# Performance work log

Hardware: AMD Instinct MI355X
Metric: run time of the kernel (lower is better)

## Reference

```python
import jax, jax.numpy as jnp
import numpy as np

B, S, D, H, HD = 2, 2048, 2048, 16, 128
MAX_TIMESCALE = 10000.0


def _fixed_pos_embedding(features, length, max_timescale):
    # flaxformer embedding.generate_fixed_pos_embedding
    fraction = jnp.arange(0, features, 2, dtype=jnp.float32) / features
    timescale = max_timescale ** fraction  # min_timescale = 1.0
    sinusoid = jnp.einsum('i,j->ij', jnp.arange(length, dtype=jnp.float32), 1.0 / timescale)
    sinusoid = jnp.concatenate([sinusoid, sinusoid], axis=-1)  # [length, features]
    return jnp.sin(sinusoid), jnp.cos(sinusoid)


def _rotate_half(x):
    x1, x2 = jnp.split(x, 2, axis=-1)
    return jnp.concatenate([-x2, x1], axis=-1)


def _apply_rope(x, sin, cos):
    # x: [B, S, H, HD]; sin/cos: [S, HD]
    sin = sin[None, :, None, :].astype(x.dtype)
    cos = cos[None, :, None, :].astype(x.dtype)
    return x * cos + _rotate_half(x) * sin


def setup_inputs() -> dict:
    key = jax.random.key(0)
    ks = jax.random.split(key, 6)
    inputs_q = jax.random.normal(ks[0], (B, S, D), dtype=jnp.float32)
    inputs_kv = jax.random.normal(ks[1], (B, S, D), dtype=jnp.float32)
    scale = D ** -0.5
    wq = jax.random.normal(ks[2], (D, H, HD), dtype=jnp.float32) * scale
    wk = jax.random.normal(ks[3], (D, H, HD), dtype=jnp.float32) * scale
    wv = jax.random.normal(ks[4], (D, H, HD), dtype=jnp.float32) * scale
    wo = jax.random.normal(ks[5], (H, HD, D), dtype=jnp.float32) * ((H * HD) ** -0.5)
    mask = jnp.tril(jnp.ones((S, S), dtype=bool))[None, None]  # causal [1,1,S,S]
    return {"inputs_q": inputs_q, "inputs_kv": inputs_kv, "wq": wq, "wk": wk,
            "wv": wv, "wo": wo, "mask": mask}


def reference(inputs_q, inputs_kv, wq, wk, wv, wo, mask):
    # QKV projections (split-head kernels) -> [B, S, H, HD]
    q = jnp.einsum('bqd,dhf->bqhf', inputs_q, wq)
    k = jnp.einsum('bkd,dhf->bkhf', inputs_kv, wk)
    v = jnp.einsum('bkd,dhf->bkhf', inputs_kv, wv)

    # Rotary embeddings applied to full head dim (fraction_to_rotate = 1.0)
    sin, cos = _fixed_pos_embedding(HD, S, MAX_TIMESCALE)
    q = _apply_rope(q, sin, cos)
    k = _apply_rope(k, sin, cos)

    # Logit rescaling by 1/sqrt(head_dim) (rescale_logits=False default path)
    q = q * (HD ** -0.5)

    logits = jnp.einsum('bqhf,bkhf->bhqk', q, k)  # [B, H, S, S]
    logits = jnp.where(mask, logits, jnp.asarray(-1e10, logits.dtype))
    probs = jax.nn.softmax(logits, axis=-1)

    ctx = jnp.einsum('bhqk,bkhf->bqhf', probs, v)
    out = jnp.einsum('bqhf,hfd->bqd', ctx, wo)  # output projection
    return out
```

## Files before the change

kernel.cpp:

```cpp
#include <hip/hip_runtime.h>

#define S_LEN 2048
#define NH 16
#define HDIM 128
#define DMODEL 2048

typedef __attribute__((ext_vector_type(8))) short bf16x8;
typedef __attribute__((ext_vector_type(4))) float f32x4;

using gas_cvp = const __attribute__((address_space(1))) void*;
using las_vp  = __attribute__((address_space(3))) void*;

__device__ __forceinline__ unsigned short f2bf(float x) {
  unsigned int u = __builtin_bit_cast(unsigned int, x);
  u += 0x7FFFu + ((u >> 16) & 1u);
  return (unsigned short)(u >> 16);
}
__device__ __forceinline__ float bf2f(unsigned short u) {
  unsigned int x = ((unsigned int)u) << 16;
  return __builtin_bit_cast(float, x);
}
__device__ __forceinline__ unsigned int cvt_pk_bf16(float lo, float hi) {
  unsigned int r;
  asm("v_cvt_pk_bf16_f32 %0, %1, %2" : "=v"(r) : "v"(lo), "v"(hi));
  return r;
}

__global__ __launch_bounds__(256) void cvt_kernel(const float4* __restrict__ in,
                                                  ushort4* __restrict__ out, int n4) {
  int i = blockIdx.x * 256 + threadIdx.x;
  if (i < n4) {
    float4 v = in[i];
    ushort4 r;
    r.x = f2bf(v.x); r.y = f2bf(v.y); r.z = f2bf(v.z); r.w = f2bf(v.w);
    out[i] = r;
  }
}

__global__ __launch_bounds__(256) void sincos_kernel(float2* __restrict__ sc) {
  int i = blockIdx.x * 256 + threadIdx.x;
  int s = i >> 6, j = i & 63;
  float inv_ts = 1.0f / powf(10000.0f, (float)j * (1.0f / 64.0f));
  float ang = (float)s * inv_ts;
  sc[i] = make_float2(sinf(ang), cosf(ang));
}

__global__ __launch_bounds__(256) void rope8_kernel(const unsigned short* __restrict__ X,
                                                    const float2* __restrict__ sc,
                                                    unsigned short* __restrict__ out,
                                                    float scale) {
  int i = blockIdx.x * 256 + threadIdx.x;
  int m = i >> 7;
  int r = i & 127;
  int h = r >> 3, jb = (r & 7) * 8;
  int s = m & (S_LEN - 1);
  size_t base = (size_t)m * DMODEL + h * HDIM + jb;
  int4 x1 = *(const int4*)(X + base);
  int4 x2 = *(const int4*)(X + base + 64);
  const float2* pp = sc + s * 64 + jb;
  int4 o1, o2;
  int* x1w = (int*)&x1; int* x2w = (int*)&x2;
  int* o1w = (int*)&o1; int* o2w = (int*)&o2;
#pragma unroll
  for (int w = 0; w < 4; w++) {
    float a_lo = bf2f((unsigned short)(x1w[w] & 0xffff));
    float a_hi = bf2f((unsigned short)((unsigned int)x1w[w] >> 16));
    float b_lo = bf2f((unsigned short)(x2w[w] & 0xffff));
    float b_hi = bf2f((unsigned short)((unsigned int)x2w[w] >> 16));
    float2 c0 = pp[w * 2], c1 = pp[w * 2 + 1];
    float r1l = (a_lo * c0.y - b_lo * c0.x) * scale;
    float r1h = (a_hi * c1.y - b_hi * c1.x) * scale;
    float r2l = (b_lo * c0.y + a_lo * c0.x) * scale;
    float r2h = (b_hi * c1.y + a_hi * c1.x) * scale;
    o1w[w] = (int)(cvt_pk_bf16(r1l, r1h));
    o2w[w] = (int)(cvt_pk_bf16(r2l, r2h));
  }
  *(int4*)(out + base) = o1;
  *(int4*)(out + base + 64) = o2;
}

__global__ __launch_bounds__(256) void wtrans_kernel(const float* __restrict__ in,
                                                     unsigned short* __restrict__ out) {
  __shared__ float tile[64][65];
  int c0 = blockIdx.x * 64, r0 = blockIdx.y * 64;
  int tx = threadIdx.x & 63, ty = threadIdx.x >> 6;
#pragma unroll
  for (int i = 0; i < 16; i++) {
    int r = ty + i * 4;
    tile[r][tx] = in[(size_t)(r0 + r) * DMODEL + c0 + tx];
  }
  __syncthreads();
#pragma unroll
  for (int i = 0; i < 16; i++) {
    int c = ty + i * 4;
    out[(size_t)(c0 + c) * DMODEL + r0 + tx] = f2bf(tile[tx][c]);
  }
}

__global__ __launch_bounds__(256) void vtrans_kernel(const unsigned short* __restrict__ vf,
                                                     unsigned short* __restrict__ Vt) {
  __shared__ unsigned short tile[64][65];
  int z = blockIdx.z; int b = z >> 4, h = z & 15;
  const unsigned short* I = vf + (size_t)b * S_LEN * DMODEL + h * HDIM;
  unsigned short* O = Vt + (size_t)z * HDIM * S_LEN;
  int s0 = blockIdx.y * 64, f0 = blockIdx.x * 64;
  int tx = threadIdx.x & 63, ty = threadIdx.x >> 6;
#pragma unroll
  for (int i = 0; i < 16; i++) {
    int r = ty + i * 4;
    tile[r][tx] = I[(size_t)(s0 + r) * DMODEL + f0 + tx];
  }
  __syncthreads();
#pragma unroll
  for (int i = 0; i < 16; i++) {
    int c = ty + i * 4;
    O[(size_t)(f0 + c) * S_LEN + s0 + tx] = tile[tx][c];
  }
}

template <bool BF16OUT>
__global__ __launch_bounds__(512) void gemm3b_kernel(
    const unsigned short* __restrict__ Aq,
    const unsigned short* __restrict__ Akv,
    const unsigned short* __restrict__ W,
    void* __restrict__ Cb) {
  constexpr int M = 4096, N = 2048, K = 2048, NT = K / 64;
  __shared__ char lds[147456];
  int z = blockIdx.z;
  const unsigned short* A = (z == 0) ? Aq : Akv;
  const unsigned short* Bt = W + (size_t)z * N * K;

  int wid = blockIdx.y * 16 + blockIdx.x;
  int nid = (wid & 7) * 32 + (wid >> 3);
  int bn = (nid & 15) * 128, bm = (nid >> 4) * 256;

  int tid = threadIdx.x, wave = tid >> 6, lane = tid & 63;
  int lr = lane & 15, lq = lane >> 4;
  int wr = wave >> 1, wc = wave & 1;

  auto STAGE_U = [&](int t, int buf, int which) {
    int k0 = (t & (NT - 1)) * 64;
    const unsigned short* src = (which < 2) ? A : Bt;
    int rbase = (which < 2) ? (bm + which * 128) : bn;
    char* dst0 = lds + buf * 49152 + which * 16384;
#pragma unroll
    for (int i = 0; i < 2; i++) {
      int o = i * 8192 + wave * 1024 + lane * 16;
      int row = o >> 7, colb = o & 127;
      int sc = colb ^ ((row & 7) << 4);
      __builtin_amdgcn_global_load_lds(
          (gas_cvp)(src + (size_t)(rbase + row) * K + k0 + (sc >> 1)),
          (las_vp)(dst0 + i * 8192 + wave * 1024), 16, 0, 0);
    }
  };
  auto LDA = [&](int buf, int m, int kk) -> bf16x8 {
    int row = wr * 64 + m * 16 + lr;
    int half = row >> 7, r = row & 127;
    int byt = r * 128 + (((kk * 4 + lq) ^ (r & 7)) << 4);
    return *(const bf16x8*)(lds + buf * 49152 + half * 16384 + byt);
  };
  auto LDB = [&](int buf, int n, int kk) -> bf16x8 {
    int row = wc * 64 + n * 16 + lr;
    int byt = row * 128 + (((kk * 4 + lq) ^ (row & 7)) << 4);
    return *(const bf16x8*)(lds + buf * 49152 + 32768 + byt);
  };

  f32x4 acc[4][4] = {};
  bf16x8 aA[2][2], bB[4][2];

  auto MFMA_H = [&](int mg) {
#pragma unroll
    for (int kk = 0; kk < 2; kk++)
#pragma unroll
      for (int mm = 0; mm < 2; mm++)
#pragma unroll
        for (int nn = 0; nn < 4; nn++)
          acc[mg * 2 + mm][nn] = __builtin_amdgcn_mfma_f32_16x16x32_bf16(
              aA[mm][kk], bB[nn][kk], acc[mg * 2 + mm][nn], 0, 0, 0);
  };
  auto PHASE_SYNC = [&]() {
    __builtin_amdgcn_s_barrier();
    asm volatile("s_waitcnt lgkmcnt(0)" ::: "memory");
    __builtin_amdgcn_sched_barrier(0);
    __builtin_amdgcn_s_setprio(1);
  };
  auto PHASE_END = [&]() {
    __builtin_amdgcn_s_setprio(0);
    __builtin_amdgcn_s_barrier();
  };

  STAGE_U(0, 0, 0); STAGE_U(0, 0, 1); STAGE_U(0, 0, 2);
  STAGE_U(1, 1, 0); STAGE_U(1, 1, 1); STAGE_U(1, 1, 2);
  asm volatile("s_waitcnt vmcnt(6)" ::: "memory");
  __builtin_amdgcn_sched_barrier(0);
  __builtin_amdgcn_s_barrier();

  int cur = 0;
  for (int T = 0; T < NT; T++) {
    int t2 = (T + 2) & (NT - 1);
    int b2 = cur + 2; if (b2 >= 3) b2 -= 3;
#pragma unroll
    for (int kk = 0; kk < 2; kk++) {
#pragma unroll
      for (int mm = 0; mm < 2; mm++) aA[mm][kk] = LDA(cur, mm, kk);
#pragma unroll
      for (int nn = 0; nn < 4; nn++) bB[nn][kk] = LDB(cur, nn, kk);
    }
    STAGE_U(t2, b2, 2); STAGE_U(t2, b2, 0);
    PHASE_SYNC(); MFMA_H(0); PHASE_END();

#pragma unroll
    for (int kk = 0; kk < 2; kk++)
#pragma unroll
      for (int mm = 0; mm < 2; mm++) aA[mm][kk] = LDA(cur, 2 + mm, kk);
    STAGE_U(t2, b2, 1);
    asm volatile("s_waitcnt vmcnt(6)" ::: "memory");
    __builtin_amdgcn_sched_barrier(0);
    PHASE_SYNC(); MFMA_H(1); PHASE_END();

    cur++; if (cur == 3) cur = 0;
  }

#pragma unroll
  for (int m = 0; m < 4; m++)
#pragma unroll
    for (int n = 0; n < 4; n++) {
      int row0 = bm + wr * 64 + m * 16 + lq * 4;
      int col = bn + wc * 64 + n * 16 + lr;
      if (BF16OUT) {
        unsigned short* C = (unsigned short*)Cb + (size_t)z * M * N;
#pragma unroll
        for (int r = 0; r < 4; r++)
          C[(size_t)(row0 + r) * N + col] = f2bf(acc[m][n][r]);
      } else {
        float* C = (float*)Cb + (size_t)z * M * N;
#pragma unroll
        for (int r = 0; r < 4; r++)
          C[(size_t)(row0 + r) * N + col] = acc[m][n][r];
      }
    }
}

__global__ __launch_bounds__(512, 1) void attn_kernel(const unsigned short* __restrict__ Qb,
                                                      const unsigned short* __restrict__ Kb,
                                                      const unsigned short* __restrict__ Vt,
                                                      unsigned short* __restrict__ ctx) {
  __shared__ char lds[65536];
  int d = blockIdx.x + 8 * (blockIdx.y + 16 * blockIdx.z);
  int jlo = (d >> 3) & 7;
  int hb = (d & 7) * 4 + (d >> 6);
  int h = hb & 15, b = hb >> 4;

  int tid = threadIdx.x, wave = tid >> 6, lane = tid & 63;
  int lr = lane & 15, lq = lane >> 4;
  int grp = wave >> 2, wsub = wave & 3;
  int qtile = grp ? (15 - jlo) : jlo;
  int qw = qtile * 128 + wsub * 32;
  int nt = 2 * (15 - jlo) + 2;

  const unsigned short* Qp = Qb + (size_t)b * S_LEN * DMODEL + (size_t)h * HDIM;
  const unsigned short* Kp = Kb + (size_t)b * S_LEN * DMODEL + (size_t)h * HDIM;
  const unsigned short* Vp = Vt + (size_t)(b * NH + h) * HDIM * S_LEN;

  bf16x8 qa[2][4];
#pragma unroll
  for (int mi = 0; mi < 2; mi++)
#pragma unroll
    for (int kf = 0; kf < 4; kf++)
      qa[mi][kf] = *(const bf16x8*)(Qp + (size_t)(qw + mi * 16 + lr) * DMODEL + kf * 32 + lq * 8);

  f32x4 o[2][8] = {};
  float mrow[2] = {-1e30f, -1e30f};
  float lsum[2] = {0.f, 0.f};

  auto STAGE = [&](int tt, int bsel) {
    int kk0 = tt * 64;
#pragma unroll
    for (int i = 0; i < 2; i++) {
      int o_ = wave * 2048 + i * 1024 + lane * 16;
      int row = o_ >> 8, colb = o_ & 255;
      int sc_ = colb ^ ((row & 7) << 4);
      __builtin_amdgcn_global_load_lds(
          (gas_cvp)(Kp + (size_t)(kk0 + row) * DMODEL + (sc_ >> 1)),
          (las_vp)(lds + bsel * 32768 + wave * 2048 + i * 1024), 16, 0, 0);
    }
#pragma unroll
    for (int i = 0; i < 2; i++) {
      int o_ = wave * 2048 + i * 1024 + lane * 16;
      int row = o_ >> 7, colb = o_ & 127;
      int sc_ = colb ^ ((row & 7) << 4);
      __builtin_amdgcn_global_load_lds(
          (gas_cvp)(Vp + (size_t)row * S_LEN + kk0 + (sc_ >> 1)),
          (las_vp)(lds + bsel * 32768 + 16384 + wave * 2048 + i * 1024), 16, 0, 0);
    }
  };

  STAGE(0, 0);
  __syncthreads();

  for (int t = 0; t < nt; t++) {
    int cur = t & 1;
    int k0 = t * 64;
    if (t + 1 < nt) STAGE(t + 1, cur ^ 1);

    bool active = (k0 <= qw + 31);
    if (active) {
      const char* kbb = lds + cur * 32768;
      f32x4 sf[2][4] = {};
#pragma unroll
      for (int kf = 0; kf < 4; kf++) {
        bf16x8 kbf[4];
#pragma unroll
        for (int nf = 0; nf < 4; nf++) {
          int row = nf * 16 + lr;
          int colb = kf * 64 + lq * 16;
          kbf[nf] = *(const bf16x8*)(kbb + row * 256 + (colb ^ ((row & 7) << 4)));
        }
#pragma unroll
        for (int nf = 0; nf < 4; nf++)
#pragma unroll
          for (int mi = 0; mi < 2; mi++)
            sf[mi][nf] = __builtin_amdgcn_mfma_f32_16x16x32_bf16(kbf[nf], qa[mi][kf], sf[mi][nf], 0, 0, 0);
      }

      if (k0 + 63 > qw) {
#pragma unroll
        for (int mi = 0; mi < 2; mi++) {
          int q = qw + mi * 16 + lr;
#pragma unroll
          for (int nf = 0; nf < 4; nf++)
#pragma unroll
            for (int r = 0; r < 4; r++)
              if (k0 + nf * 16 + lq * 4 + r > q) sf[mi][nf][r] = -1e30f;
        }
      }

      float vmax[2];
#pragma unroll
      for (int mi = 0; mi < 2; mi++) {
        float v = sf[mi][0][0];
#pragma unroll
        for (int nf = 0; nf < 4; nf++)
#pragma unroll
          for (int r = 0; r < 4; r++) v = fmaxf(v, sf[mi][nf][r]);
        v = fmaxf(v, __shfl_xor(v, 16));
        v = fmaxf(v, __shfl_xor(v, 32));
        vmax[mi] = v;
      }
      bool need = (vmax[0] > mrow[0] + 8.f) || (vmax[1] > mrow[1] + 8.f);
      if (__any(need)) {
#pragma unroll
        for (int mi = 0; mi < 2; mi++) {
          float mn = fmaxf(mrow[mi], vmax[mi]);
          float al = __expf(mrow[mi] - mn);
          mrow[mi] = mn;
          lsum[mi] *= al;
#pragma unroll
          for (int ff = 0; ff < 8; ff++) o[mi][ff] *= al;
        }
      }
#pragma unroll
      for (int mi = 0; mi < 2; mi++) {
        float rs = 0.f;
#pragma unroll
        for (int nf = 0; nf < 4; nf++)
#pragma unroll
          for (int r = 0; r < 4; r++) {
            float p = __expf(sf[mi][nf][r] - mrow[mi]);
            sf[mi][nf][r] = p;
            rs += p;
          }
        rs += __shfl_xor(rs, 16);
        rs += __shfl_xor(rs, 32);
        lsum[mi] += rs;
      }

      const char* vbb = lds + cur * 32768 + 16384;
      bool hi = (lane >= 32);
      bool odd = (lq & 1);
#pragma unroll
      for (int c = 0; c < 2; c++) {
        bf16x8 pfrag[2];
#pragma unroll
        for (int mi = 0; mi < 2; mi++) {
          unsigned int A0 = cvt_pk_bf16(sf[mi][2 * c][0], sf[mi][2 * c][1]);
          unsigned int A1 = cvt_pk_bf16(sf[mi][2 * c][2], sf[mi][2 * c][3]);
          unsigned int B0 = cvt_pk_bf16(sf[mi][2 * c + 1][0], sf[mi][2 * c + 1][1]);
          unsigned int B1 = cvt_pk_bf16(sf[mi][2 * c + 1][2], sf[mi][2 * c + 1][3]);
          unsigned int sA0 = (unsigned int)__shfl_xor((int)A0, 32);
          unsigned int sA1 = (unsigned int)__shfl_xor((int)A1, 32);
          unsigned int sB0 = (unsigned int)__shfl_xor((int)B0, 32);
          unsigned int sB1 = (unsigned int)__shfl_xor((int)B1, 32);
          unsigned int Y0f = hi ? sB0 : A0, Y0s = hi ? B0 : sA0;
          unsigned int Y1f = hi ? sB1 : A1, Y1s = hi ? B1 : sA1;
          unsigned int z0 = odd ? Y0f : Y0s, z1 = odd ? Y1f : Y1s;
          unsigned int w0 = (unsigned int)__shfl_xor((int)z0, 16);
          unsigned int w1 = (unsigned int)__shfl_xor((int)z1, 16);
          int4 fr;
          fr.x = (int)(odd ? w0 : Y0f);
          fr.y = (int)(odd ? w1 : Y1f);
          fr.z = (int)(odd ? Y0s : w0);
          fr.w = (int)(odd ? Y1s : w1);
          pfrag[mi] = __builtin_bit_cast(bf16x8, fr);
        }
#pragma unroll
        for (int ff = 0; ff < 8; ff++) {
          int row = ff * 16 + lr;
          int colb = c * 64 + lq * 16;
          bf16x8 vb = *(const bf16x8*)(vbb + row * 128 + (colb ^ ((row & 7) << 4)));
#pragma unroll
          for (int mi = 0; mi < 2; mi++)
            o[mi][ff] = __builtin_amdgcn_mfma_f32_16x16x32_bf16(vb, pfrag[mi], o[mi][ff], 0, 0, 0);
        }
      }
    }

    __syncthreads();
  }

#pragma unroll
  for (int mi = 0; mi < 2; mi++) {
    float inv = 1.0f / lsum[mi];
    size_t rb = ((size_t)b * S_LEN + qw + mi * 16 + lr) * DMODEL + h * HDIM;
#pragma unroll
    for (int ff = 0; ff < 8; ff++) {
      unsigned int u0 = cvt_pk_bf16(o[mi][ff][0] * inv, o[mi][ff][1] * inv);
      unsigned int u1 = cvt_pk_bf16(o[mi][ff][2] * inv, o[mi][ff][3] * inv);
      *(uint2*)(ctx + rb + ff * 16 + lq * 4) = make_uint2(u0, u1);
    }
  }
}

extern "C" void kernel_launch(void* const* d_in, const int* in_sizes, int n_in,
                              void* d_out, int out_size, void* d_ws, size_t ws_size,
                              hipStream_t stream) {
  const float* inq  = (const float*)d_in[0];
  const float* inkv = (const float*)d_in[1];
  const float* wq   = (const float*)d_in[2];
  const float* wk   = (const float*)d_in[3];
  const float* wv   = (const float*)d_in[4];
  const float* wo   = (const float*)d_in[5];
  float* out = (float*)d_out;

  char* ws = (char*)d_ws;
  const size_t MB = 1ull << 20;
  unsigned short* xq  = (unsigned short*)(ws);
  unsigned short* xkv = (unsigned short*)(ws + 16 * MB);
  unsigned short* wqt = (unsigned short*)(ws + 32 * MB);
  unsigned short* wkt = (unsigned short*)(ws + 40 * MB);
  unsigned short* wvt = (unsigned short*)(ws + 48 * MB);
  unsigned short* wot = (unsigned short*)(ws + 56 * MB);
  float2* sc          = (float2*)(ws + 64 * MB);
  unsigned short* projb = (unsigned short*)(ws + 66 * MB);
  unsigned short* Vt   = (unsigned short*)(ws + 114 * MB);
  unsigned short* ctxb = (unsigned short*)(ws + 130 * MB);
  unsigned short* Qb = xq;
  unsigned short* Kb = xkv;

  const int n4 = (2 * S_LEN * DMODEL) / 4;
  cvt_kernel<<<n4 / 256, 256, 0, stream>>>((const float4*)inq, (ushort4*)xq, n4);
  cvt_kernel<<<n4 / 256, 256, 0, stream>>>((const float4*)inkv, (ushort4*)xkv, n4);

  dim3 tg(32, 32);
  wtrans_kernel<<<tg, 256, 0, stream>>>(wq, wqt);
  wtrans_kernel<<<tg, 256, 0, stream>>>(wk, wkt);
  wtrans_kernel<<<tg, 256, 0, stream>>>(wv, wvt);
  wtrans_kernel<<<tg, 256, 0, stream>>>(wo, wot);

  sincos_kernel<<<(S_LEN * 64) / 256, 256, 0, stream>>>(sc);

  const float qscale = 0.08838834764831845f;
  unsigned short* projQ = projb;
  unsigned short* projK = projb + (size_t)4096 * 2048;
  unsigned short* projV = projb + (size_t)2 * 4096 * 2048;

  gemm3b_kernel<true><<<dim3(16, 16, 3), 512, 0, stream>>>(xq, xkv, wqt, (void*)projb);

  rope8_kernel<<<2048, 256, 0, stream>>>(projQ, sc, Qb, qscale);
  rope8_kernel<<<2048, 256, 0, stream>>>(projK, sc, Kb, 1.0f);
  vtrans_kernel<<<dim3(2, 32, 32), 256, 0, stream>>>(projV, Vt);

  attn_kernel<<<dim3(8, NH, 2), 512, 0, stream>>>(Qb, Kb, Vt, ctxb);

  gemm3b_kernel<false><<<dim3(16, 16, 1), 512, 0, stream>>>(ctxb, ctxb, wot, (void*)out);
}
```

Before: 297.4 us.

## Enlarge GEMM tile to 256x256 with double-buffered quarter-phase pipeline and merge small launches

The projection GEMM moves from 256x128 tiles with a triple buffer to 256x256 tiles with a double buffer. Each wave now computes a 128x64 sub-tile in four MFMA quarter phases, and global-to-LDS staging is interleaved between those phases. The aim is more arithmetic per byte loaded, at the cost of more accumulator registers and fewer blocks. The four weight-transpose launches are merged into one grid-z launch, and the two RoPE launches into one, to cut launch overhead.

Result: no change. 302.0 us (+1.6%).

```diff
diff --git a/kernel.cpp b/kernel.cpp
--- a/kernel.cpp
+++ b/kernel.cpp
@@ -45,10 +45,15 @@
   sc[i] = make_float2(sinf(ang), cosf(ang));
 }
 
-__global__ __launch_bounds__(256) void rope8_kernel(const unsigned short* __restrict__ X,
+__global__ __launch_bounds__(256) void rope8_kernel(const unsigned short* __restrict__ XQ,
+                                                    const unsigned short* __restrict__ XK,
                                                     const float2* __restrict__ sc,
-                                                    unsigned short* __restrict__ out,
-                                                    float scale) {
+                                                    unsigned short* __restrict__ outQ,
+                                                    unsigned short* __restrict__ outK,
+                                                    float qscale) {
+  const unsigned short* X = blockIdx.z ? XK : XQ;
+  unsigned short* out = blockIdx.z ? outK : outQ;
+  float scale = blockIdx.z ? 1.0f : qscale;
   int i = blockIdx.x * 256 + threadIdx.x;
   int m = i >> 7;
   int r = i & 127;
@@ -79,9 +84,15 @@
   *(int4*)(out + base + 64) = o2;
 }
 
-__global__ __launch_bounds__(256) void wtrans_kernel(const float* __restrict__ in,
-                                                     unsigned short* __restrict__ out) {
+__global__ __launch_bounds__(256) void wtrans4_kernel(const float* __restrict__ w0,
+                                                      const float* __restrict__ w1,
+                                                      const float* __restrict__ w2,
+                                                      const float* __restrict__ w3,
+                                                      unsigned short* __restrict__ outb) {
   __shared__ float tile[64][65];
+  int z = blockIdx.z;
+  const float* in = (z == 0) ? w0 : (z == 1) ? w1 : (z == 2) ? w2 : w3;
+  unsigned short* out = outb + (size_t)z * DMODEL * DMODEL;
   int c0 = blockIdx.x * 64, r0 = blockIdx.y * 64;
   int tx = threadIdx.x & 63, ty = threadIdx.x >> 6;
 #pragma unroll
@@ -119,113 +130,134 @@
 }
 
 template <bool BF16OUT>
-__global__ __launch_bounds__(512) void gemm3b_kernel(
+__global__ __launch_bounds__(512, 2) void gemm256_kernel(
     const unsigned short* __restrict__ Aq,
     const unsigned short* __restrict__ Akv,
     const unsigned short* __restrict__ W,
     void* __restrict__ Cb) {
   constexpr int M = 4096, N = 2048, K = 2048, NT = K / 64;
-  __shared__ char lds[147456];
+  __shared__ char lds[131072];
   int z = blockIdx.z;
   const unsigned short* A = (z == 0) ? Aq : Akv;
   const unsigned short* Bt = W + (size_t)z * N * K;
 
-  int wid = blockIdx.y * 16 + blockIdx.x;
-  int nid = (wid & 7) * 32 + (wid >> 3);
-  int bn = (nid & 15) * 128, bm = (nid >> 4) * 256;
+  int wid = blockIdx.y * 8 + blockIdx.x;
+  int nid = (wid & 7) * 16 + (wid >> 3);
+  int bn = (nid & 7) * 256, bm = (nid >> 3) * 256;
 
   int tid = threadIdx.x, wave = tid >> 6, lane = tid & 63;
   int lr = lane & 15, lq = lane >> 4;
-  int wr = wave >> 1, wc = wave & 1;
-
-  auto STAGE_U = [&](int t, int buf, int which) {
+  int wr = wave >> 2, wc = wave & 3;
+
+  auto STAGE_Q = [&](int t, int buf, int isB, int q) {
     int k0 = (t & (NT - 1)) * 64;
-    const unsigned short* src = (which < 2) ? A : Bt;
-    int rbase = (which < 2) ? (bm + which * 128) : bn;
-    char* dst0 = lds + buf * 49152 + which * 16384;
-#pragma unroll
-    for (int i = 0; i < 2; i++) {
-      int o = i * 8192 + wave * 1024 + lane * 16;
-      int row = o >> 7, colb = o & 127;
-      int sc = colb ^ ((row & 7) << 4);
-      __builtin_amdgcn_global_load_lds(
-          (gas_cvp)(src + (size_t)(rbase + row) * K + k0 + (sc >> 1)),
-          (las_vp)(dst0 + i * 8192 + wave * 1024), 16, 0, 0);
-    }
-  };
+    const unsigned short* src = isB ? Bt : A;
+    int rbase = (isB ? bn : bm) + q * 64;
+    int o = tid * 16;
+    int row = o >> 7, colb = o & 127;
+    int sc = colb ^ ((row & 7) << 4);
+    __builtin_amdgcn_global_load_lds(
+        (gas_cvp)(src + (size_t)(rbase + row) * K + k0 + (sc >> 1)),
+        (las_vp)(lds + buf * 65536 + isB * 32768 + (q >> 1) * 16384 + (q & 1) * 8192 + wave * 1024),
+        16, 0, 0);
+  };
+  auto STAGE_AA = [&](int t, int buf) { STAGE_Q(t, buf, 0, 0); STAGE_Q(t, buf, 0, 2); };
+  auto STAGE_BIG = [&](int t, int buf) {
+    STAGE_Q(t, buf, 0, 1); STAGE_Q(t, buf, 0, 3);
+    STAGE_Q(t, buf, 1, 0); STAGE_Q(t, buf, 1, 1);
+    STAGE_Q(t, buf, 1, 2); STAGE_Q(t, buf, 1, 3);
+  };
+
   auto LDA = [&](int buf, int m, int kk) -> bf16x8 {
-    int row = wr * 64 + m * 16 + lr;
+    int row = wr * 128 + m * 16 + lr;
     int half = row >> 7, r = row & 127;
-    int byt = r * 128 + (((kk * 4 + lq) ^ (r & 7)) << 4);
-    return *(const bf16x8*)(lds + buf * 49152 + half * 16384 + byt);
+    return *(const bf16x8*)(lds + buf * 65536 + half * 16384 + r * 128 +
+                            (((kk * 4 + lq) ^ (r & 7)) << 4));
   };
   auto LDB = [&](int buf, int n, int kk) -> bf16x8 {
     int row = wc * 64 + n * 16 + lr;
-    int byt = row * 128 + (((kk * 4 + lq) ^ (row & 7)) << 4);
-    return *(const bf16x8*)(lds + buf * 49152 + 32768 + byt);
-  };
-
-  f32x4 acc[4][4] = {};
-  bf16x8 aA[2][2], bB[4][2];
-
-  auto MFMA_H = [&](int mg) {
+    int half = row >> 7, r = row & 127;
+    return *(const bf16x8*)(lds + buf * 65536 + 32768 + half * 16384 + r * 128 +
+                            (((kk * 4 + lq) ^ (r & 7)) << 4));
+  };
+
+  f32x4 acc[8][4] = {};
+  bf16x8 aA[4][2], bB[4][2];
+
+  auto DS_A = [&](int buf, int mg) {
 #pragma unroll
     for (int kk = 0; kk < 2; kk++)
 #pragma unroll
-      for (int mm = 0; mm < 2; mm++)
-#pragma unroll
-        for (int nn = 0; nn < 4; nn++)
-          acc[mg * 2 + mm][nn] = __builtin_amdgcn_mfma_f32_16x16x32_bf16(
-              aA[mm][kk], bB[nn][kk], acc[mg * 2 + mm][nn], 0, 0, 0);
-  };
-  auto PHASE_SYNC = [&]() {
+      for (int mm = 0; mm < 4; mm++) aA[mm][kk] = LDA(buf, mg * 4 + mm, kk);
+  };
+  auto DS_B = [&](int buf, int ng) {
+#pragma unroll
+    for (int kk = 0; kk < 2; kk++)
+#pragma unroll
+      for (int nn = 0; nn < 2; nn++) bB[ng * 2 + nn][kk] = LDB(buf, ng * 2 + nn, kk);
+  };
+  auto MFMA_Q = [&](int mg, int ng) {
+#pragma unroll
+    for (int kk = 0; kk < 2; kk++)
+#pragma unroll
+      for (int mm = 0; mm < 4; mm++)
+#pragma unroll
+        for (int nn = 0; nn < 2; nn++)
+          acc[mg * 4 + mm][ng * 2 + nn] = __builtin_amdgcn_mfma_f32_16x16x32_bf16(
+              aA[mm][kk], bB[ng * 2 + nn][kk], acc[mg * 4 + mm][ng * 2 + nn], 0, 0, 0);
+  };
+  auto PH_MID = [&]() {
     __builtin_amdgcn_s_barrier();
     asm volatile("s_waitcnt lgkmcnt(0)" ::: "memory");
     __builtin_amdgcn_sched_barrier(0);
     __builtin_amdgcn_s_setprio(1);
   };
-  auto PHASE_END = [&]() {
+  auto PH_ENDP = [&]() {
     __builtin_amdgcn_s_setprio(0);
     __builtin_amdgcn_s_barrier();
   };
-
-  STAGE_U(0, 0, 0); STAGE_U(0, 0, 1); STAGE_U(0, 0, 2);
-  STAGE_U(1, 1, 0); STAGE_U(1, 1, 1); STAGE_U(1, 1, 2);
-  asm volatile("s_waitcnt vmcnt(6)" ::: "memory");
+  auto PH_END_VM2 = [&]() {
+    __builtin_amdgcn_s_setprio(0);
+    asm volatile("s_waitcnt vmcnt(2)" ::: "memory");
+    __builtin_amdgcn_sched_barrier(0);
+    __builtin_amdgcn_s_barrier();
+  };
+
+  STAGE_AA(0, 0); STAGE_BIG(0, 0);
+  STAGE_AA(1, 1);
+  asm volatile("s_waitcnt vmcnt(2)" ::: "memory");
   __builtin_amdgcn_sched_barrier(0);
   __builtin_amdgcn_s_barrier();
 
-  int cur = 0;
-  for (int T = 0; T < NT; T++) {
-    int t2 = (T + 2) & (NT - 1);
-    int b2 = cur + 2; if (b2 >= 3) b2 -= 3;
-#pragma unroll
-    for (int kk = 0; kk < 2; kk++) {
-#pragma unroll
-      for (int mm = 0; mm < 2; mm++) aA[mm][kk] = LDA(cur, mm, kk);
-#pragma unroll
-      for (int nn = 0; nn < 4; nn++) bB[nn][kk] = LDB(cur, nn, kk);
-    }
-    STAGE_U(t2, b2, 2); STAGE_U(t2, b2, 0);
-    PHASE_SYNC(); MFMA_H(0); PHASE_END();
-
-#pragma unroll
-    for (int kk = 0; kk < 2; kk++)
-#pragma unroll
-      for (int mm = 0; mm < 2; mm++) aA[mm][kk] = LDA(cur, 2 + mm, kk);
-    STAGE_U(t2, b2, 1);
-    asm volatile("s_waitcnt vmcnt(6)" ::: "memory");
-    __builtin_amdgcn_sched_barrier(0);
-    PHASE_SYNC(); MFMA_H(1); PHASE_END();
-
-    cur++; if (cur == 3) cur = 0;
-  }
-
-#pragma unroll
-  for (int m = 0; m < 4; m++)
+  for (int i = 0; i < NT / 2; i++) {
+    int T = 2 * i, U = T + 1;
+    int t2 = (T + 2) & (NT - 1), u2 = (U + 2) & (NT - 1);
+    DS_A(0, 0); DS_B(0, 0);
+    STAGE_BIG(U, 1);
+    PH_MID(); MFMA_Q(0, 0); PH_ENDP();
+    DS_B(0, 1);
+    PH_MID(); MFMA_Q(0, 1); PH_ENDP();
+    DS_A(0, 1);
+    STAGE_AA(t2, 0);
+    PH_MID(); MFMA_Q(1, 0); PH_ENDP();
+    PH_MID(); MFMA_Q(1, 1); PH_END_VM2();
+    DS_A(1, 0); DS_B(1, 0);
+    STAGE_BIG(t2, 0);
+    PH_MID(); MFMA_Q(0, 0); PH_ENDP();
+    DS_B(1, 1);
+    PH_MID(); MFMA_Q(0, 1); PH_ENDP();
+    DS_A(1, 1);
+    STAGE_AA(u2, 1);
+    PH_MID(); MFMA_Q(1, 0); PH_ENDP();
+    PH_MID(); MFMA_Q(1, 1); PH_END_VM2();
+  }
+  asm volatile("s_waitcnt vmcnt(0)" ::: "memory");
+
+#pragma unroll
+  for (int m = 0; m < 8; m++)
 #pragma unroll
     for (int n = 0; n < 4; n++) {
-      int row0 = bm + wr * 64 + m * 16 + lq * 4;
+      int row0 = bm + wr * 128 + m * 16 + lq * 4;
       int col = bn + wc * 64 + n * 16 + lr;
       if (BF16OUT) {
         unsigned short* C = (unsigned short*)Cb + (size_t)z * M * N;
@@ -447,8 +479,6 @@
   unsigned short* xq  = (unsigned short*)(ws);
   unsigned short* xkv = (unsigned short*)(ws + 16 * MB);
   unsigned short* wqt = (unsigned short*)(ws + 32 * MB);
-  unsigned short* wkt = (unsigned short*)(ws + 40 * MB);
-  unsigned short* wvt = (unsigned short*)(ws + 48 * MB);
   unsigned short* wot = (unsigned short*)(ws + 56 * MB);
   float2* sc          = (float2*)(ws + 64 * MB);
   unsigned short* projb = (unsigned short*)(ws + 66 * MB);
@@ -461,11 +491,7 @@
   cvt_kernel<<<n4 / 256, 256, 0, stream>>>((const float4*)inq, (ushort4*)xq, n4);
   cvt_kernel<<<n4 / 256, 256, 0, stream>>>((const float4*)inkv, (ushort4*)xkv, n4);
 
-  dim3 tg(32, 32);
-  wtrans_kernel<<<tg, 256, 0, stream>>>(wq, wqt);
-  wtrans_kernel<<<tg, 256, 0, stream>>>(wk, wkt);
-  wtrans_kernel<<<tg, 256, 0, stream>>>(wv, wvt);
-  wtrans_kernel<<<tg, 256, 0, stream>>>(wo, wot);
+  wtrans4_kernel<<<dim3(32, 32, 4), 256, 0, stream>>>(wq, wk, wv, wo, wqt);
 
   sincos_kernel<<<(S_LEN * 64) / 256, 256, 0, stream>>>(sc);
 
@@ -474,13 +500,12 @@
   unsigned short* projK = projb + (size_t)4096 * 2048;
   unsigned short* projV = projb + (size_t)2 * 4096 * 2048;
 
-  gemm3b_kernel<true><<<dim3(16, 16, 3), 512, 0, stream>>>(xq, xkv, wqt, (void*)projb);
-
-  rope8_kernel<<<2048, 256, 0, stream>>>(projQ, sc, Qb, qscale);
-  rope8_kernel<<<2048, 256, 0, stream>>>(projK, sc, Kb, 1.0f);
+  gemm256_kernel<true><<<dim3(8, 16, 3), 512, 0, stream>>>(xq, xkv, wqt, (void*)projb);
+
+  rope8_kernel<<<dim3(2048, 1, 2), 256, 0, stream>>>(projQ, projK, sc, Qb, Kb, qscale);
   vtrans_kernel<<<dim3(2, 32, 32), 256, 0, stream>>>(projV, Vt);
 
   attn_kernel<<<dim3(8, NH, 2), 512, 0, stream>>>(Qb, Kb, Vt, ctxb);
 
-  gemm3b_kernel<false><<<dim3(16, 16, 1), 512, 0, stream>>>(ctxb, ctxb, wot, (void*)out);
-}
+  gemm256_kernel<false><<<dim3(8, 16, 1), 512, 0, stream>>>(ctxb, ctxb, wot, (void*)out);
+}
```

## Use 256x256-tile ping-pong GEMM for QKV projection and merge small launches

Applied to the files above, without the earlier changes.

Replaces the 256x128-tile QKV projection GEMM with a new 256x256-tile kernel. The new kernel double-buffers global-to-LDS loads, interleaves LDS fragment reads with MFMA quadrants, and raises wave priority around the MFMA phases, so each block does more compute per byte loaded. It also merges the four weight-transpose launches into one launch over blockIdx.z and the two RoPE launches into one, cutting launch overhead. The larger tile yields 384 blocks instead of 768, which may hurt load balance, and the heavier per-thread accumulator state adds register pressure. The output-projection GEMM is unchanged.

Result: faster. 285.2 us (-4.1%).

```diff
diff --git a/kernel.cpp b/kernel.cpp
--- a/kernel.cpp
+++ b/kernel.cpp
@@ -45,10 +45,15 @@
   sc[i] = make_float2(sinf(ang), cosf(ang));
 }
 
-__global__ __launch_bounds__(256) void rope8_kernel(const unsigned short* __restrict__ X,
+__global__ __launch_bounds__(256) void rope8_kernel(const unsigned short* __restrict__ XQ,
+                                                    const unsigned short* __restrict__ XK,
                                                     const float2* __restrict__ sc,
-                                                    unsigned short* __restrict__ out,
-                                                    float scale) {
+                                                    unsigned short* __restrict__ outQ,
+                                                    unsigned short* __restrict__ outK,
+                                                    float qscale) {
+  const unsigned short* X = blockIdx.z ? XK : XQ;
+  unsigned short* out = blockIdx.z ? outK : outQ;
+  float scale = blockIdx.z ? 1.0f : qscale;
   int i = blockIdx.x * 256 + threadIdx.x;
   int m = i >> 7;
   int r = i & 127;
@@ -79,9 +84,15 @@
   *(int4*)(out + base + 64) = o2;
 }
 
-__global__ __launch_bounds__(256) void wtrans_kernel(const float* __restrict__ in,
-                                                     unsigned short* __restrict__ out) {
+__global__ __launch_bounds__(256) void wtrans4_kernel(const float* __restrict__ w0,
+                                                      const float* __restrict__ w1,
+                                                      const float* __restrict__ w2,
+                                                      const float* __restrict__ w3,
+                                                      unsigned short* __restrict__ outb) {
   __shared__ float tile[64][65];
+  int z = blockIdx.z;
+  const float* in = (z == 0) ? w0 : (z == 1) ? w1 : (z == 2) ? w2 : w3;
+  unsigned short* out = outb + (size_t)z * DMODEL * DMODEL;
   int c0 = blockIdx.x * 64, r0 = blockIdx.y * 64;
   int tx = threadIdx.x & 63, ty = threadIdx.x >> 6;
 #pragma unroll
@@ -116,6 +127,170 @@
     int c = ty + i * 4;
     O[(size_t)(f0 + c) * S_LEN + s0 + tx] = tile[tx][c];
   }
+}
+
+template <bool BF16OUT>
+__global__ __launch_bounds__(512, 2) void gemm256v2_kernel(
+    const unsigned short* __restrict__ Aq,
+    const unsigned short* __restrict__ Akv,
+    const unsigned short* __restrict__ W,
+    void* __restrict__ Cb) {
+  constexpr int M = 4096, N = 2048, K = 2048, NT = K / 64;
+  __shared__ char lds[131072];
+  int z = blockIdx.z;
+  const unsigned short* A = (z == 0) ? Aq : Akv;
+  const unsigned short* Bt = W + (size_t)z * N * K;
+
+  int wid = blockIdx.y * 8 + blockIdx.x;
+  int nid = (wid & 7) * 16 + (wid >> 3);
+  int bn = (nid & 7) * 256, bm = (nid >> 3) * 256;
+
+  int tid = threadIdx.x, wave = tid >> 6, lane = tid & 63;
+  int lr = lane & 15, lq = lane >> 4;
+  int wr = wave >> 2, wc = wave & 3;
+
+  auto STAGE_H = [&](int t, int buf, int isB, int h) {
+    int k0 = (t & (NT - 1)) * 64;
+    const unsigned short* src = isB ? Bt : A;
+    int rbase = (isB ? bn : bm) + h * 128;
+    char* dst0 = lds + buf * 65536 + isB * 32768 + h * 16384;
+#pragma unroll
+    for (int i = 0; i < 2; i++) {
+      int o = i * 8192 + tid * 16;
+      int row = o >> 7, colb = o & 127;
+      int sc = colb ^ ((row & 7) << 4);
+      __builtin_amdgcn_global_load_lds(
+          (gas_cvp)(src + (size_t)(rbase + row) * K + k0 + (sc >> 1)),
+          (las_vp)(dst0 + i * 8192 + wave * 1024), 16, 0, 0);
+    }
+  };
+
+  auto LDA = [&](int buf, int m, int kk) -> bf16x8 {
+    int row = wr * 128 + m * 16 + lr;
+    int half = row >> 7, r = row & 127;
+    return *(const bf16x8*)(lds + buf * 65536 + half * 16384 + r * 128 +
+                            (((kk * 4 + lq) ^ (r & 7)) << 4));
+  };
+  auto LDB = [&](int buf, int n, int kk) -> bf16x8 {
+    int row = wc * 64 + n * 16 + lr;
+    int half = row >> 7, r = row & 127;
+    return *(const bf16x8*)(lds + buf * 65536 + 32768 + half * 16384 + r * 128 +
+                            (((kk * 4 + lq) ^ (r & 7)) << 4));
+  };
+
+  f32x4 acc[8][4] = {};
+  bf16x8 aA[4][2], bN0[2][2], bN1[2][2];
+
+  auto Q_mg0_n0 = [&]() {
+#pragma unroll
+    for (int kk = 0; kk < 2; kk++)
+#pragma unroll
+      for (int mm = 0; mm < 4; mm++)
+#pragma unroll
+        for (int nn = 0; nn < 2; nn++)
+          acc[mm][nn] = __builtin_amdgcn_mfma_f32_16x16x32_bf16(aA[mm][kk], bN0[nn][kk], acc[mm][nn], 0, 0, 0);
+  };
+  auto Q_mg0_n1 = [&]() {
+#pragma unroll
+    for (int kk = 0; kk < 2; kk++)
+#pragma unroll
+      for (int mm = 0; mm < 4; mm++)
+#pragma unroll
+        for (int nn = 0; nn < 2; nn++)
+          acc[mm][2 + nn] = __builtin_amdgcn_mfma_f32_16x16x32_bf16(aA[mm][kk], bN1[nn][kk], acc[mm][2 + nn], 0, 0, 0);
+  };
+  auto Q_mg1_n0 = [&]() {
+#pragma unroll
+    for (int kk = 0; kk < 2; kk++)
+#pragma unroll
+      for (int mm = 0; mm < 4; mm++)
+#pragma unroll
+        for (int nn = 0; nn < 2; nn++)
+          acc[4 + mm][nn] = __builtin_amdgcn_mfma_f32_16x16x32_bf16(aA[mm][kk], bN0[nn][kk], acc[4 + mm][nn], 0, 0, 0);
+  };
+  auto Q_mg1_n1 = [&]() {
+#pragma unroll
+    for (int kk = 0; kk < 2; kk++)
+#pragma unroll
+      for (int mm = 0; mm < 4; mm++)
+#pragma unroll
+        for (int nn = 0; nn < 2; nn++)
+          acc[4 + mm][2 + nn] = __builtin_amdgcn_mfma_f32_16x16x32_bf16(aA[mm][kk], bN1[nn][kk], acc[4 + mm][2 + nn], 0, 0, 0);
+  };
+
+  auto PH_MID = [&]() {
+    __builtin_amdgcn_s_barrier();
+    asm volatile("s_waitcnt lgkmcnt(0)" ::: "memory");
+    __builtin_amdgcn_sched_barrier(0);
+    __builtin_amdgcn_s_setprio(1);
+  };
+  auto PH_ENDP = [&]() {
+    __builtin_amdgcn_s_setprio(0);
+    __builtin_amdgcn_s_barrier();
+  };
+
+  STAGE_H(0, 0, 0, 0); STAGE_H(0, 0, 0, 1); STAGE_H(0, 0, 1, 0); STAGE_H(0, 0, 1, 1);
+  STAGE_H(1, 1, 1, 0); STAGE_H(1, 1, 1, 1);
+  asm volatile("s_waitcnt vmcnt(4)" ::: "memory");
+  __builtin_amdgcn_sched_barrier(0);
+  __builtin_amdgcn_s_barrier();
+
+  for (int X = 0; X < NT; X++) {
+    int c = X & 1, nc = c ^ 1;
+#pragma unroll
+    for (int kk = 0; kk < 2; kk++)
+#pragma unroll
+      for (int nn = 0; nn < 2; nn++) bN0[nn][kk] = LDB(c, nn, kk);
+    STAGE_H(X + 1, nc, 0, 0);
+    PH_MID();
+    if (X) Q_mg1_n1();
+    PH_ENDP();
+
+#pragma unroll
+    for (int kk = 0; kk < 2; kk++)
+#pragma unroll
+      for (int mm = 0; mm < 4; mm++) aA[mm][kk] = LDA(c, mm, kk);
+    STAGE_H(X + 1, nc, 0, 1);
+    PH_MID(); Q_mg0_n0(); PH_ENDP();
+
+#pragma unroll
+    for (int kk = 0; kk < 2; kk++)
+#pragma unroll
+      for (int nn = 0; nn < 2; nn++) bN1[nn][kk] = LDB(c, 2 + nn, kk);
+    PH_MID(); Q_mg0_n1(); PH_ENDP();
+
+#pragma unroll
+    for (int kk = 0; kk < 2; kk++)
+#pragma unroll
+      for (int mm = 0; mm < 4; mm++) aA[mm][kk] = LDA(c, 4 + mm, kk);
+    STAGE_H(X + 2, c, 1, 0); STAGE_H(X + 2, c, 1, 1);
+    PH_MID(); Q_mg1_n0();
+    __builtin_amdgcn_s_setprio(0);
+    asm volatile("s_waitcnt vmcnt(4)" ::: "memory");
+    __builtin_amdgcn_sched_barrier(0);
+    __builtin_amdgcn_s_barrier();
+  }
+  Q_mg1_n1();
+  asm volatile("s_waitcnt vmcnt(0)" ::: "memory");
+
+#pragma unroll
+  for (int m = 0; m < 8; m++)
+#pragma unroll
+    for (int n = 0; n < 4; n++) {
+      int row0 = bm + wr * 128 + m * 16 + lq * 4;
+      int col = bn + wc * 64 + n * 16 + lr;
+      if (BF16OUT) {
+        unsigned short* C = (unsigned short*)Cb + (size_t)z * M * N;
+#pragma unroll
+        for (int r = 0; r < 4; r++)
+          C[(size_t)(row0 + r) * N + col] = f2bf(acc[m][n][r]);
+      } else {
+        float* C = (float*)Cb + (size_t)z * M * N;
+#pragma unroll
+        for (int r = 0; r < 4; r++)
+          C[(size_t)(row0 + r) * N + col] = acc[m][n][r];
+      }
+    }
 }
 
 template <bool BF16OUT>
@@ -447,8 +622,6 @@
   unsigned short* xq  = (unsigned short*)(ws);
   unsigned short* xkv = (unsigned short*)(ws + 16 * MB);
   unsigned short* wqt = (unsigned short*)(ws + 32 * MB);
-  unsigned short* wkt = (unsigned short*)(ws + 40 * MB);
-  unsigned short* wvt = (unsigned short*)(ws + 48 * MB);
   unsigned short* wot = (unsigned short*)(ws + 56 * MB);
   float2* sc          = (float2*)(ws + 64 * MB);
   unsigned short* projb = (unsigned short*)(ws + 66 * MB);
@@ -461,11 +634,7 @@
   cvt_kernel<<<n4 / 256, 256, 0, stream>>>((const float4*)inq, (ushort4*)xq, n4);
   cvt_kernel<<<n4 / 256, 256, 0, stream>>>((const float4*)inkv, (ushort4*)xkv, n4);
 
-  dim3 tg(32, 32);
-  wtrans_kernel<<<tg, 256, 0, stream>>>(wq, wqt);
-  wtrans_kernel<<<tg, 256, 0, stream>>>(wk, wkt);
-  wtrans_kernel<<<tg, 256, 0, stream>>>(wv, wvt);
-  wtrans_kernel<<<tg, 256, 0, stream>>>(wo, wot);
+  wtrans4_kernel<<<dim3(32, 32, 4), 256, 0, stream>>>(wq, wk, wv, wo, wqt);
 
   sincos_kernel<<<(S_LEN * 64) / 256, 256, 0, stream>>>(sc);
 
@@ -474,10 +643,9 @@
   unsigned short* projK = projb + (size_t)4096 * 2048;
   unsigned short* projV = projb + (size_t)2 * 4096 * 2048;
 
-  gemm3b_kernel<true><<<dim3(16, 16, 3), 512, 0, stream>>>(xq, xkv, wqt, (void*)projb);
-
-  rope8_kernel<<<2048, 256, 0, stream>>>(projQ, sc, Qb, qscale);
-  rope8_kernel<<<2048, 256, 0, stream>>>(projK, sc, Kb, 1.0f);
+  gemm256v2_kernel<true><<<dim3(8, 16, 3), 512, 0, stream>>>(xq, xkv, wqt, (void*)projb);
+
+  rope8_kernel<<<dim3(2048, 1, 2), 256, 0, stream>>>(projQ, projK, sc, Qb, Kb, qscale);
   vtrans_kernel<<<dim3(2, 32, 32), 256, 0, stream>>>(projV, Vt);
 
   attn_kernel<<<dim3(8, NH, 2), 512, 0, stream>>>(Qb, Kb, Vt, ctxb);
```

## Restructure GEMM main loop pipeline and batch weight-transpose and RoPE launches

Applied to the files above, without the earlier changes.

The GEMM main loop is rewritten so each K-step issues all three next-tile prefetches up front. It then loads A and B fragments in staggered groups and runs MFMA quadrants behind partial lgkmcnt waits, which drops one barrier pair per iteration and peels the last two iterations so no wrapped tiles are prefetched. The four weight-transpose launches and the two RoPE launches are each merged into one grid-z-indexed launch to cut launch overhead. Risks include heavier register pressure, since all A fragments are now held, and fragile waitcnt accounting.

New measurement: 283.9 us. 1.05x faster.

```diff
diff --git a/kernel.cpp b/kernel.cpp
--- a/kernel.cpp
+++ b/kernel.cpp
@@ -45,10 +45,15 @@
   sc[i] = make_float2(sinf(ang), cosf(ang));
 }
 
-__global__ __launch_bounds__(256) void rope8_kernel(const unsigned short* __restrict__ X,
+__global__ __launch_bounds__(256) void rope8_kernel(const unsigned short* __restrict__ XQ,
+                                                    const unsigned short* __restrict__ XK,
                                                     const float2* __restrict__ sc,
-                                                    unsigned short* __restrict__ out,
-                                                    float scale) {
+                                                    unsigned short* __restrict__ outQ,
+                                                    unsigned short* __restrict__ outK,
+                                                    float qscale) {
+  const unsigned short* X = blockIdx.z ? XK : XQ;
+  unsigned short* out = blockIdx.z ? outK : outQ;
+  float scale = blockIdx.z ? 1.0f : qscale;
   int i = blockIdx.x * 256 + threadIdx.x;
   int m = i >> 7;
   int r = i & 127;
@@ -79,9 +84,15 @@
   *(int4*)(out + base + 64) = o2;
 }
 
-__global__ __launch_bounds__(256) void wtrans_kernel(const float* __restrict__ in,
-                                                     unsigned short* __restrict__ out) {
+__global__ __launch_bounds__(256) void wtrans4_kernel(const float* __restrict__ w0,
+                                                      const float* __restrict__ w1,
+                                                      const float* __restrict__ w2,
+                                                      const float* __restrict__ w3,
+                                                      unsigned short* __restrict__ outb) {
   __shared__ float tile[64][65];
+  int z = blockIdx.z;
+  const float* in = (z == 0) ? w0 : (z == 1) ? w1 : (z == 2) ? w2 : w3;
+  unsigned short* out = outb + (size_t)z * DMODEL * DMODEL;
   int c0 = blockIdx.x * 64, r0 = blockIdx.y * 64;
   int tx = threadIdx.x & 63, ty = threadIdx.x >> 6;
 #pragma unroll
@@ -119,7 +130,7 @@
 }
 
 template <bool BF16OUT>
-__global__ __launch_bounds__(512) void gemm3b_kernel(
+__global__ __launch_bounds__(512, 1) void gemmk_kernel(
     const unsigned short* __restrict__ Aq,
     const unsigned short* __restrict__ Akv,
     const unsigned short* __restrict__ W,
@@ -139,7 +150,7 @@
   int wr = wave >> 1, wc = wave & 1;
 
   auto STAGE_U = [&](int t, int buf, int which) {
-    int k0 = (t & (NT - 1)) * 64;
+    int k0 = t * 64;
     const unsigned short* src = (which < 2) ? A : Bt;
     int rbase = (which < 2) ? (bm + which * 128) : bn;
     char* dst0 = lds + buf * 49152 + which * 16384;
@@ -166,60 +177,80 @@
   };
 
   f32x4 acc[4][4] = {};
-  bf16x8 aA[2][2], bB[4][2];
-
-  auto MFMA_H = [&](int mg) {
+  bf16x8 aA[4][2], bB[4][2];
+
+  auto QUAD = [&](int mg, int ng) {
 #pragma unroll
     for (int kk = 0; kk < 2; kk++)
 #pragma unroll
       for (int mm = 0; mm < 2; mm++)
 #pragma unroll
-        for (int nn = 0; nn < 4; nn++)
-          acc[mg * 2 + mm][nn] = __builtin_amdgcn_mfma_f32_16x16x32_bf16(
-              aA[mm][kk], bB[nn][kk], acc[mg * 2 + mm][nn], 0, 0, 0);
+        for (int nn = 0; nn < 2; nn++)
+          acc[mg * 2 + mm][ng * 2 + nn] = __builtin_amdgcn_mfma_f32_16x16x32_bf16(
+              aA[mg * 2 + mm][kk], bB[ng * 2 + nn][kk], acc[mg * 2 + mm][ng * 2 + nn], 0, 0, 0);
   };
-  auto PHASE_SYNC = [&]() {
+
+  auto BODY = [&](int T, int cur, int dst, int mode) {
     __builtin_amdgcn_s_barrier();
+    if (mode == 0) {
+      STAGE_U(T + 2, dst, 0); STAGE_U(T + 2, dst, 1); STAGE_U(T + 2, dst, 2);
+    }
+    __builtin_amdgcn_sched_barrier(0);
+#pragma unroll
+    for (int kk = 0; kk < 2; kk++)
+#pragma unroll
+      for (int mm = 0; mm < 2; mm++) aA[mm][kk] = LDA(cur, mm, kk);
+#pragma unroll
+    for (int kk = 0; kk < 2; kk++)
+#pragma unroll
+      for (int nn = 0; nn < 2; nn++) bB[nn][kk] = LDB(cur, nn, kk);
+    __builtin_amdgcn_sched_barrier(0);
+#pragma unroll
+    for (int kk = 0; kk < 2; kk++)
+#pragma unroll
+      for (int nn = 0; nn < 2; nn++) bB[2 + nn][kk] = LDB(cur, 2 + nn, kk);
+    __builtin_amdgcn_sched_barrier(0);
+#pragma unroll
+    for (int kk = 0; kk < 2; kk++)
+#pragma unroll
+      for (int mm = 0; mm < 2; mm++) aA[2 + mm][kk] = LDA(cur, 2 + mm, kk);
+    __builtin_amdgcn_sched_barrier(0);
+
+    asm volatile("s_waitcnt lgkmcnt(8)" ::: "memory");
+    __builtin_amdgcn_sched_barrier(0);
+    __builtin_amdgcn_s_setprio(1);
+    QUAD(0, 0);
+    __builtin_amdgcn_s_setprio(0);
+    asm volatile("s_waitcnt lgkmcnt(4)" ::: "memory");
+    __builtin_amdgcn_sched_barrier(0);
+    __builtin_amdgcn_s_setprio(1);
+    QUAD(0, 1);
+    __builtin_amdgcn_s_setprio(0);
     asm volatile("s_waitcnt lgkmcnt(0)" ::: "memory");
     __builtin_amdgcn_sched_barrier(0);
     __builtin_amdgcn_s_setprio(1);
-  };
-  auto PHASE_END = [&]() {
+    QUAD(1, 0); QUAD(1, 1);
     __builtin_amdgcn_s_setprio(0);
-    __builtin_amdgcn_s_barrier();
+    if (mode == 0)      asm volatile("s_waitcnt vmcnt(6)" ::: "memory");
+    else if (mode == 1) asm volatile("s_waitcnt vmcnt(0)" ::: "memory");
+    __builtin_amdgcn_sched_barrier(0);
   };
 
   STAGE_U(0, 0, 0); STAGE_U(0, 0, 1); STAGE_U(0, 0, 2);
   STAGE_U(1, 1, 0); STAGE_U(1, 1, 1); STAGE_U(1, 1, 2);
   asm volatile("s_waitcnt vmcnt(6)" ::: "memory");
   __builtin_amdgcn_sched_barrier(0);
-  __builtin_amdgcn_s_barrier();
 
   int cur = 0;
-  for (int T = 0; T < NT; T++) {
-    int t2 = (T + 2) & (NT - 1);
-    int b2 = cur + 2; if (b2 >= 3) b2 -= 3;
-#pragma unroll
-    for (int kk = 0; kk < 2; kk++) {
-#pragma unroll
-      for (int mm = 0; mm < 2; mm++) aA[mm][kk] = LDA(cur, mm, kk);
-#pragma unroll
-      for (int nn = 0; nn < 4; nn++) bB[nn][kk] = LDB(cur, nn, kk);
-    }
-    STAGE_U(t2, b2, 2); STAGE_U(t2, b2, 0);
-    PHASE_SYNC(); MFMA_H(0); PHASE_END();
-
-#pragma unroll
-    for (int kk = 0; kk < 2; kk++)
-#pragma unroll
-      for (int mm = 0; mm < 2; mm++) aA[mm][kk] = LDA(cur, 2 + mm, kk);
-    STAGE_U(t2, b2, 1);
-    asm volatile("s_waitcnt vmcnt(6)" ::: "memory");
-    __builtin_amdgcn_sched_barrier(0);
-    PHASE_SYNC(); MFMA_H(1); PHASE_END();
-
-    cur++; if (cur == 3) cur = 0;
-  }
+  for (int T = 0; T < NT - 2; T++) {
+    int dst = (cur == 0) ? 2 : cur - 1;
+    BODY(T, cur, dst, 0);
+    cur = (cur == 2) ? 0 : cur + 1;
+  }
+  BODY(NT - 2, cur, 0, 1);
+  cur = (cur == 2) ? 0 : cur + 1;
+  BODY(NT - 1, cur, 0, 2);
+  asm volatile("s_waitcnt vmcnt(0) lgkmcnt(0)" ::: "memory");
 
 #pragma unroll
   for (int m = 0; m < 4; m++)
@@ -447,8 +478,6 @@
   unsigned short* xq  = (unsigned short*)(ws);
   unsigned short* xkv = (unsigned short*)(ws + 16 * MB);
   unsigned short* wqt = (unsigned short*)(ws + 32 * MB);
-  unsigned short* wkt = (unsigned short*)(ws + 40 * MB);
-  unsigned short* wvt = (unsigned short*)(ws + 48 * MB);
   unsigned short* wot = (unsigned short*)(ws + 56 * MB);
   float2* sc          = (float2*)(ws + 64 * MB);
   unsigned short* projb = (unsigned short*)(ws + 66 * MB);
@@ -461,11 +490,7 @@
   cvt_kernel<<<n4 / 256, 256, 0, stream>>>((const float4*)inq, (ushort4*)xq, n4);
   cvt_kernel<<<n4 / 256, 256, 0, stream>>>((const float4*)inkv, (ushort4*)xkv, n4);
 
-  dim3 tg(32, 32);
-  wtrans_kernel<<<tg, 256, 0, stream>>>(wq, wqt);
-  wtrans_kernel<<<tg, 256, 0, stream>>>(wk, wkt);
-  wtrans_kernel<<<tg, 256, 0, stream>>>(wv, wvt);
-  wtrans_kernel<<<tg, 256, 0, stream>>>(wo, wot);
+  wtrans4_kernel<<<dim3(32, 32, 4), 256, 0, stream>>>(wq, wk, wv, wo, wqt);
 
   sincos_kernel<<<(S_LEN * 64) / 256, 256, 0, stream>>>(sc);
 
@@ -474,13 +499,12 @@
   unsigned short* projK = projb + (size_t)4096 * 2048;
   unsigned short* projV = projb + (size_t)2 * 4096 * 2048;
 
-  gemm3b_kernel<true><<<dim3(16, 16, 3), 512, 0, stream>>>(xq, xkv, wqt, (void*)projb);
-
-  rope8_kernel<<<2048, 256, 0, stream>>>(projQ, sc, Qb, qscale);
-  rope8_kernel<<<2048, 256, 0, stream>>>(projK, sc, Kb, 1.0f);
+  gemmk_kernel<true><<<dim3(16, 16, 3), 512, 0, stream>>>(xq, xkv, wqt, (void*)projb);
+
+  rope8_kernel<<<dim3(2048, 1, 2), 256, 0, stream>>>(projQ, projK, sc, Qb, Kb, qscale);
   vtrans_kernel<<<dim3(2, 32, 32), 256, 0, stream>>>(projV, Vt);
 
   attn_kernel<<<dim3(8, NH, 2), 512, 0, stream>>>(Qb, Kb, Vt, ctxb);
 
-  gemm3b_kernel<false><<<dim3(16, 16, 1), 512, 0, stream>>>(ctxb, ctxb, wot, (void*)out);
-}
+  gemmk_kernel<false><<<dim3(16, 16, 1), 512, 0, stream>>>(ctxb, ctxb, wot, (void*)out);
+}
```
